# Optimization experiments

Hardware: AMD Instinct MI355X
Metric: run time of the kernel (lower is better)

The kernel has to match this reference:

```python
import jax, jax.numpy as jnp
import numpy as np

B, S, D, H = 2, 4096, 512, 8
HD = D // H  # head_dim = 64


def setup_inputs() -> dict:
    key = jax.random.key(0)
    ks = jax.random.split(key, 7)
    scale = 1.0 / np.sqrt(D)
    return {
        "x": jax.random.normal(ks[0], (B, S, D), dtype=jnp.float32),
        "Wq": jax.random.uniform(ks[1], (D, D), jnp.float32, -scale, scale),
        "bq": jax.random.uniform(ks[2], (D,), jnp.float32, -scale, scale),
        "Wk": jax.random.uniform(ks[3], (D, D), jnp.float32, -scale, scale),
        "bk": jax.random.uniform(ks[4], (D,), jnp.float32, -scale, scale),
        "Wv": jax.random.uniform(ks[5], (D, D), jnp.float32, -scale, scale),
        "bv": jax.random.uniform(ks[6], (D,), jnp.float32, -scale, scale),
    }


def reference(x, Wq, bq, Wk, bk, Wv, bv):
    # torch Linear: y = x @ W.T + b
    q = x @ Wq.T + bq  # [B,S,D]
    k = x @ Wk.T + bk
    v = x @ Wv.T + bv
    # split heads -> [B,H,S,HD]
    q = q.reshape(B, S, H, HD).transpose(0, 2, 1, 3)
    k = k.reshape(B, S, H, HD).transpose(0, 2, 1, 3)
    v = v.reshape(B, S, H, HD).transpose(0, 2, 1, 3)
    # NOTE: module scales by sqrt(pitch_dim), NOT sqrt(head_dim) -- keep faithful.
    scores = jnp.einsum("bhqd,bhkd->bhqk", q, k) / jnp.sqrt(jnp.float32(D))
    causal = jnp.tril(jnp.ones((S, S), dtype=bool))  # lower-tri incl. diag allowed
    scores = jnp.where(causal, scores, -jnp.inf)
    attn = jax.nn.softmax(scores, axis=-1)
    out = jnp.einsum("bhqk,bhkd->bhqd", attn, v)  # [B,H,S,HD]
    return out.transpose(0, 2, 1, 3).reshape(B, S, D)
```

## Files before the change

kernel.cpp:

```cpp
#include <hip/hip_runtime.h>
#include <hip/hip_bf16.h>
#include <math.h>

#define BB 2
#define SS 4096
#define DD 512
#define HH 8
#define HD 64
#define MSD (BB*SS*DD)
#define WSZ (DD*DD)

#define XOFF (4*(size_t)MSD)
#define WOFF (5*(size_t)MSD)
#define POFF (3*(size_t)MSD)

typedef __attribute__((ext_vector_type(8))) short bf16x8;
typedef __attribute__((ext_vector_type(4))) float f32x4;

__device__ __forceinline__ unsigned short f2bf(float f) {
    unsigned int u = __float_as_uint(f);
    u += 0x7fff + ((u >> 16) & 1);
    return (unsigned short)(u >> 16);
}
__device__ __forceinline__ unsigned int pk2bf(float a, float b) {
    __hip_bfloat162 h = __float22bfloat162_rn(make_float2(a, b));
    union { __hip_bfloat162 h2; unsigned int u; } cv; cv.h2 = h;
    return cv.u;
}

#define GLD16(gsrc, ldst) \
    __builtin_amdgcn_global_load_lds((const __attribute__((address_space(1))) unsigned int*)(gsrc), \
                                     (__attribute__((address_space(3))) unsigned int*)(ldst), 16, 0, 0)

#define CH(qb,t0,t1) ((unsigned)(qb) | ((unsigned)(t0)<<8) | ((unsigned)(t1)<<16))
__device__ __constant__ unsigned int SCHED[48] = {
  CH(31,0,32),  CH(31,32,64), CH(0,0,2),
  CH(15,0,32),  CH(29,0,30),  CH(1,0,4),
  CH(29,30,60), CH(14,0,30),  CH(2,0,6),
  CH(28,0,29),  CH(28,29,58), CH(3,0,8),
  CH(27,0,28),  CH(13,0,28),  CH(4,0,10),
  CH(26,0,27),  CH(26,27,54), CH(5,0,12),
  CH(25,0,26),  CH(12,0,26),  CH(6,0,14),
  CH(24,0,25),  CH(24,25,50), CH(7,0,16),
  CH(30,0,31),  CH(17,0,18),  CH(16,0,17),
  CH(30,31,62), CH(17,18,36), CH(16,17,34),
  CH(27,28,56), CH(19,0,20),  CH(8,0,18),
  CH(25,26,52), CH(20,0,21),  CH(18,0,19),
  CH(23,0,24),  CH(22,0,23),  CH(18,19,38),
  CH(23,24,48), CH(21,0,22),  CH(19,20,40),
  CH(11,0,24),  CH(21,22,44), CH(9,0,20),
  CH(22,23,46), CH(10,0,22),  CH(20,21,42),
};

__global__ __launch_bounds__(256)
void convert_bf16(const float* __restrict__ x,
                  const float* __restrict__ Wq, const float* __restrict__ Wk,
                  const float* __restrict__ Wv, unsigned short* __restrict__ ws) {
    const int i8 = blockIdx.x*256 + threadIdx.x;
    const float* src; unsigned short* dst; size_t off;
    if (i8 < MSD/8) {
        src = x; dst = ws + XOFF; off = (size_t)i8 * 8;
    } else {
        size_t o = ((size_t)i8 - MSD/8) * 8;
        int wsel = (int)(o / WSZ);
        src = (wsel == 0) ? Wq : (wsel == 1) ? Wk : Wv;
        dst = ws + WOFF + (size_t)wsel*WSZ;
        off = o % WSZ;
    }
    float4 a = *(const float4*)&src[off];
    float4 b = *(const float4*)&src[off+4];
    unsigned short r[8] = { f2bf(a.x), f2bf(a.y), f2bf(a.z), f2bf(a.w),
                            f2bf(b.x), f2bf(b.y), f2bf(b.z), f2bf(b.w) };
    *(bf16x8*)&dst[off] = *(const bf16x8*)r;
}

__global__ __launch_bounds__(512, 2)
void qkv_fused(const float* __restrict__ bq, const float* __restrict__ bk,
               const float* __restrict__ bv, unsigned short* __restrict__ ws) {
    const unsigned short* Xb = ws + XOFF;
    const unsigned short* Wz0 = ws + WOFF;
    const unsigned short* Wz1 = ws + WOFF + WSZ;
    const unsigned short* Wz2 = ws + WOFF + 2*(size_t)WSZ;

    __shared__ __align__(16) unsigned short As[2][128*64];
    __shared__ __align__(16) unsigned short Bs[3][2][128*64];

    const int tid  = threadIdx.x;
    const int w    = tid >> 6, l = tid & 63;
    const int quad = l >> 4,  r16 = l & 15;
    const int wm   = w >> 2,  wn  = w & 3;
    const int n0   = blockIdx.x * 128;
    const int m0   = blockIdx.y * 128;

    const int sr8 = l >> 3, sc = l & 7;

    f32x4 acc[3][4][2];
    #pragma unroll
    for (int z = 0; z < 3; ++z)
        #pragma unroll
        for (int i = 0; i < 4; ++i)
            #pragma unroll
            for (int j = 0; j < 2; ++j) acc[z][i][j] = (f32x4){0.f,0.f,0.f,0.f};

    auto STAGE = [&](int k0, int b) {
        #pragma unroll
        for (int u = 0; u < 2; ++u) {
            const int r0  = w*16 + u*8;
            const int row = r0 + sr8;
            const int c   = sc ^ (row & 7);
            GLD16(&Xb [(size_t)(m0 + row)*DD + k0 + c*8], &As[b][r0*64]);
            GLD16(&Wz0[(size_t)(n0 + row)*DD + k0 + c*8], &Bs[0][b][r0*64]);
            GLD16(&Wz1[(size_t)(n0 + row)*DD + k0 + c*8], &Bs[1][b][r0*64]);
            GLD16(&Wz2[(size_t)(n0 + row)*DD + k0 + c*8], &Bs[2][b][r0*64]);
        }
    };

    STAGE(0, 0);

    #pragma unroll
    for (int kt = 0; kt < 8; ++kt) {
        __syncthreads();
        if (kt + 1 < 8) STAGE((kt + 1)*64, (kt + 1) & 1);

        const int bb = kt & 1;
        #pragma unroll
        for (int kc = 0; kc < 2; ++kc) {
            bf16x8 a[4];
            #pragma unroll
            for (int i = 0; i < 4; ++i) {
                const int mr = wm*64 + i*16 + r16;
                a[i] = *(const bf16x8*)&As[bb][mr*64 + (((kc*4+quad) ^ (mr&7))*8)];
            }
            bf16x8 b0[2], b1[2], b2[2];
            #pragma unroll
            for (int j = 0; j < 2; ++j) {
                const int nr = wn*32 + j*16 + r16;
                const int sw = ((kc*4+quad) ^ (nr&7))*8;
                b0[j] = *(const bf16x8*)&Bs[0][bb][nr*64 + sw];
                b1[j] = *(const bf16x8*)&Bs[1][bb][nr*64 + sw];
                b2[j] = *(const bf16x8*)&Bs[2][bb][nr*64 + sw];
            }
            __builtin_amdgcn_s_setprio(1);
            #pragma unroll
            for (int i = 0; i < 4; ++i)
                #pragma unroll
                for (int j = 0; j < 2; ++j) {
                    acc[0][i][j] = __builtin_amdgcn_mfma_f32_16x16x32_bf16(b0[j], a[i], acc[0][i][j], 0, 0, 0);
                    acc[1][i][j] = __builtin_amdgcn_mfma_f32_16x16x32_bf16(b1[j], a[i], acc[1][i][j], 0, 0, 0);
                    acc[2][i][j] = __builtin_amdgcn_mfma_f32_16x16x32_bf16(a[i], b2[j], acc[2][i][j], 0, 0, 0);
                }
            __builtin_amdgcn_s_setprio(0);
        }
    }

    __syncthreads();
    unsigned short* Ct = &As[0][0];
    const float qscale = 0.04419417382415922f * 1.4426950408889634f;
    const float* biases[3] = { bq, bk, bv };

    #pragma unroll
    for (int z = 0; z < 3; ++z) {
        unsigned short* dst = ws + (size_t)z*MSD;
        const float* bias = biases[z];

        if (z == 2) {
            #pragma unroll
            for (int j = 0; j < 2; ++j) {
                const int nloc = wn*32 + j*16 + r16;
                const float bz = bias[n0 + nloc];
                #pragma unroll
                for (int i = 0; i < 4; ++i) {
                    const int chunk = wm*8 + i*2 + (quad>>1);
                    const int off   = (quad & 1) * 4;
                    unsigned short r4[4];
                    #pragma unroll
                    for (int reg = 0; reg < 4; ++reg)
                        r4[reg] = f2bf(acc[2][i][j][reg] + bz);
                    *(uint2*)&Ct[nloc*128 + ((chunk ^ (nloc & 7))*8) + off] = *(const uint2*)r4;
                }
            }
        } else {
            #pragma unroll
            for (int j = 0; j < 2; ++j) {
                const int nbase = wn*32 + j*16 + quad*4;
                const float4 bz4 = *(const float4*)&bias[n0 + nbase];
                const int chunk = wn*4 + j*2 + (quad>>1);
                const int off   = (quad & 1) * 4;
                #pragma unroll
                for (int i = 0; i < 4; ++i) {
                    const int mloc = wm*64 + i*16 + r16;
                    float v0 = acc[z][i][j][0] + bz4.x;
                    float v1 = acc[z][i][j][1] + bz4.y;
                    float v2 = acc[z][i][j][2] + bz4.z;
                    float v3 = acc[z][i][j][3] + bz4.w;
                    if (z == 0) { v0 *= qscale; v1 *= qscale; v2 *= qscale; v3 *= qscale; }
                    unsigned short r4[4] = { f2bf(v0), f2bf(v1), f2bf(v2), f2bf(v3) };
                    *(uint2*)&Ct[mloc*128 + ((chunk ^ (mloc & 7))*8) + off] = *(const uint2*)r4;
                }
            }
        }
        __syncthreads();

        if (z == 2) {
            const int b_ = m0 >> 12, s0_ = m0 & (SS-1);
            #pragma unroll
            for (int p = 0; p < 4; ++p) {
                const int f = p*512 + tid;
                const int nrow = f >> 4;
                const int mch  = f & 15;
                bf16x8 v = *(const bf16x8*)&Ct[nrow*128 + ((mch ^ (nrow & 7))*8)];
                const int ng = n0 + nrow;
                const int h = ng >> 6, hd = ng & 63;
                *(bf16x8*)&dst[((size_t)(b_*HH + h)*HD + hd)*SS + s0_ + mch*8] = v;
            }
        } else {
            #pragma unroll
            for (int p = 0; p < 4; ++p) {
                const int f = p*512 + tid;
                const int hh  = f >> 10;
                const int rem = f & 1023;
                const int sr  = rem >> 3;
                const int ch  = rem & 7;
                bf16x8 v = *(const bf16x8*)&Ct[sr*128 + (((hh*8 + ch) ^ (sr & 7))*8)];
                const int mg = m0 + sr;
                const int b_ = mg >> 12, s_ = mg & (SS-1);
                const int hg = (n0 >> 6) + hh;
                *(bf16x8*)&dst[((size_t)(b_*HH + hg)*SS + s_)*HD + ch*8] = v;
            }
        }
        if (z < 2) __syncthreads();
    }
}

__global__ __launch_bounds__(512, 6)
void attn_mfma(unsigned short* __restrict__ ws, float* __restrict__ out) {
    const int bx = blockIdx.x;
    const int k_ = bx >> 8;
    const int j_ = bx & 255;
    const int bh = j_ & 15;
    const int ti = j_ >> 4;
    const unsigned int e = SCHED[ti*3 + k_];
    const int qb = e & 255;
    const int t0 = (e >> 8) & 255;
    const int t1 = (e >> 16) & 255;
    const int split = !(t0 == 0 && t1 == 2*qb + 2);
    const int half  = (t0 != 0);

    const int tid  = threadIdx.x;
    const int w    = tid >> 6, l = tid & 63;
    const int quad = l >> 4,  r16 = l & 15;
    const int qlo  = qb*128 + w*16;
    const int tdiag = 2*qb + (w >> 2);
    const int qoff  = (w & 3)*16;

    const unsigned short* Qg  = ws;
    const unsigned short* Kg  = ws + (size_t)MSD;
    const unsigned short* Vtg = ws + 2*(size_t)MSD;

    __shared__ __align__(16) unsigned short Ks[2][64*64];
    __shared__ __align__(16) unsigned short Vs[2][64*64];

    const size_t kbase = (size_t)bh*SS*HD;
    const size_t vbase = (size_t)bh*HD*SS;

    bf16x8 bqf[2];
    #pragma unroll
    for (int kc = 0; kc < 2; ++kc)
        bqf[kc] = *(const bf16x8*)&Qg[kbase + (size_t)(qlo + r16)*HD + kc*32 + quad*8];

    const f32x4 ZZ = (f32x4){0.f,0.f,0.f,0.f};
    const unsigned short onep[8] = {0x3F80,0x3F80,0x3F80,0x3F80,0x3F80,0x3F80,0x3F80,0x3F80};
    const bf16x8 ones8 = *(const bf16x8*)onep;

    f32x4 od[4];
    #pragma unroll
    for (int mt = 0; mt < 4; ++mt) od[mt] = ZZ;
    f32x4 lacc = ZZ;

    const int sr8 = l >> 3, sc = l & 7;
    const int srow = w*8 + sr8;
    const int scol = sc ^ (srow & 7);

    {
        const int jb0 = t0*64;
        GLD16(&Kg [kbase + (size_t)(jb0 + srow)*HD + scol*8], &Ks[0][(w*8)*64]);
        GLD16(&Vtg[vbase + (size_t)srow*SS + jb0 + scol*8],   &Vs[0][(w*8)*64]);
    }

    for (int t = t0; t < t1; ++t) {
        __syncthreads();

        if (t + 1 < t1) {
            const int jb1 = (t + 1)*64;
            const int b1  = (t + 1 - t0) & 1;
            GLD16(&Kg [kbase + (size_t)(jb1 + srow)*HD + scol*8], &Ks[b1][(w*8)*64]);
            GLD16(&Vtg[vbase + (size_t)srow*SS + jb1 + scol*8],   &Vs[b1][(w*8)*64]);
        }

        if (t <= tdiag) {
            const int bc = (t - t0) & 1;
            const unsigned short* Kb = Ks[bc];
            const unsigned short* Vb = Vs[bc];

            f32x4 z[4];
            __builtin_amdgcn_s_setprio(1);
            #pragma unroll
            for (int mt = 0; mt < 4; ++mt) {
                const int row = mt*16 + r16;
                bf16x8 ak0 = *(const bf16x8*)&Kb[row*64 + ((quad     ^ (row&7))*8)];
                bf16x8 ak1 = *(const bf16x8*)&Kb[row*64 + (((4+quad) ^ (row&7))*8)];
                z[mt] = __builtin_amdgcn_mfma_f32_16x16x32_bf16(ak0, bqf[0], ZZ, 0, 0, 0);
                z[mt] = __builtin_amdgcn_mfma_f32_16x16x32_bf16(ak1, bqf[1], z[mt], 0, 0, 0);
            }
            __builtin_amdgcn_s_setprio(0);

            if (t == tdiag) {
                #pragma unroll
                for (int mt = 0; mt < 4; ++mt)
                    #pragma unroll
                    for (int reg = 0; reg < 4; ++reg)
                        if (mt*16 + quad*4 + reg > qoff + r16)
                            z[mt][reg] = -1e30f;
            }

            unsigned int X0[4], X1[4];
            #pragma unroll
            for (int mt = 0; mt < 4; ++mt) {
                X0[mt] = pk2bf(__builtin_amdgcn_exp2f(z[mt][0]),
                               __builtin_amdgcn_exp2f(z[mt][1]));
                X1[mt] = pk2bf(__builtin_amdgcn_exp2f(z[mt][2]),
                               __builtin_amdgcn_exp2f(z[mt][3]));
            }

            bf16x8 pf[2];
            #pragma unroll
            for (int kc = 0; kc < 2; ++kc) {
                unsigned int a0 = X0[2*kc], b0 = X0[2*kc+1];
                unsigned int a1 = X1[2*kc], b1 = X1[2*kc+1];
                asm("v_permlane32_swap_b32 %0, %1" : "+v"(a0), "+v"(b0));
                asm("v_permlane16_swap_b32 %0, %1" : "+v"(a0), "+v"(b0));
                asm("v_permlane32_swap_b32 %0, %1" : "+v"(a1), "+v"(b1));
                asm("v_permlane16_swap_b32 %0, %1" : "+v"(a1), "+v"(b1));
                unsigned int wv[4] = { a0, a1, b0, b1 };
                pf[kc] = *(const bf16x8*)wv;
            }

            __builtin_amdgcn_s_setprio(1);
            lacc = __builtin_amdgcn_mfma_f32_16x16x32_bf16(ones8, pf[0], lacc, 0, 0, 0);
            lacc = __builtin_amdgcn_mfma_f32_16x16x32_bf16(ones8, pf[1], lacc, 0, 0, 0);
            #pragma unroll
            for (int mt = 0; mt < 4; ++mt) {
                const int row = mt*16 + r16;
                bf16x8 av0 = *(const bf16x8*)&Vb[row*64 + ((quad     ^ (row&7))*8)];
                bf16x8 av1 = *(const bf16x8*)&Vb[row*64 + (((4+quad) ^ (row&7))*8)];
                od[mt] = __builtin_amdgcn_mfma_f32_16x16x32_bf16(av0, pf[0], od[mt], 0, 0, 0);
                od[mt] = __builtin_amdgcn_mfma_f32_16x16x32_bf16(av1, pf[1], od[mt], 0, 0, 0);
            }
            __builtin_amdgcn_s_setprio(0);
        }
    }

    if (split) {
        const int p = 2*(bh*16 + (qb - 16)) + half;
        float* Op = (float*)(ws + POFF) + (size_t)p*(128*64);
        float* Lp = (float*)(ws + WOFF) + p*128;
        const int qloc = w*16 + r16;
        if (quad == 0) Lp[qloc] = lacc[0];
        #pragma unroll
        for (int mt = 0; mt < 4; ++mt)
            *(f32x4*)&Op[(size_t)qloc*64 + mt*16 + quad*4] = od[mt];
    } else {
        const int b_ = bh >> 3, h = bh & 7;
        const float inv = 1.0f / lacc[0];
        const int q = qlo + r16;
        float* op = out + ((size_t)(b_*SS + q))*DD + h*HD;
        #pragma unroll
        for (int mt = 0; mt < 4; ++mt) {
            float4 tt;
            tt.x = od[mt][0]*inv; tt.y = od[mt][1]*inv;
            tt.z = od[mt][2]*inv; tt.w = od[mt][3]*inv;
            *(float4*)&op[mt*16 + quad*4] = tt;
        }
    }
}

__global__ __launch_bounds__(256)
void attn_combine(const unsigned short* __restrict__ ws, float* __restrict__ out) {
    const int i  = blockIdx.x*256 + threadIdx.x;
    const int d4 = i & 15;
    const int q  = (i >> 4) & 127;
    const int r  = i >> 11;
    const int bh = r >> 4, qb = 16 + (r & 15);

    const float* Opart = (const float*)(ws + POFF);
    const float* Lpart = (const float*)(ws + WOFF);

    const float4 a = *(const float4*)&Opart[((size_t)(2*r)*128 + q)*64 + d4*4];
    const float4 b = *(const float4*)&Opart[((size_t)(2*r + 1)*128 + q)*64 + d4*4];
    const float lt = Lpart[(2*r)*128 + q] + Lpart[(2*r + 1)*128 + q];
    const float inv = 1.0f / lt;

    const int qg = qb*128 + q;
    const int b_ = bh >> 3, h = bh & 7;
    float4 o;
    o.x = (a.x + b.x)*inv; o.y = (a.y + b.y)*inv;
    o.z = (a.z + b.z)*inv; o.w = (a.w + b.w)*inv;
    *(float4*)&out[((size_t)(b_*SS + qg))*DD + h*HD + d4*4] = o;
}

extern "C" void kernel_launch(void* const* d_in, const int* in_sizes, int n_in,
                              void* d_out, int out_size, void* d_ws, size_t ws_size,
                              hipStream_t stream) {
    const float* x  = (const float*)d_in[0];
    const float* Wq = (const float*)d_in[1];
    const float* bq = (const float*)d_in[2];
    const float* Wk = (const float*)d_in[3];
    const float* bk = (const float*)d_in[4];
    const float* Wv = (const float*)d_in[5];
    const float* bv = (const float*)d_in[6];
    float* out = (float*)d_out;
    unsigned short* ws = (unsigned short*)d_ws;

    const int nconv = (MSD/8 + 3*WSZ/8 + 255) / 256;
    convert_bf16<<<nconv, 256, 0, stream>>>(x, Wq, Wk, Wv, ws);

    dim3 ggrid(DD/128, (BB*SS)/128);
    qkv_fused<<<ggrid, 512, 0, stream>>>(bq, bk, bv, ws);

    attn_mfma<<<768, 512, 0, stream>>>(ws, out);
    attn_combine<<<2048, 256, 0, stream>>>(ws, out);
}
```

Baseline: 152.2 us.

## Give each attention wave two query tiles and halve block size to 256

The attention kernel now uses 4 waves per block instead of 8, and each wave handles 32 query rows as two 16-row tiles instead of one. Each K and V fragment read from LDS is reused for two MFMA tiles, which halves LDS reads per FLOP, and each thread issues two global-to-LDS loads per tile. The cost is more accumulator and P registers per wave and fewer waves to hide latency. The launch bounds change to 256 threads with a minimum of 4 blocks per CU.

```diff
diff --git a/kernel.cpp b/kernel.cpp
--- a/kernel.cpp
+++ b/kernel.cpp
@@ -232,7 +232,7 @@
     }
 }
 
-__global__ __launch_bounds__(512, 6)
+__global__ __launch_bounds__(256, 4)
 void attn_mfma(unsigned short* __restrict__ ws, float* __restrict__ out) {
     const int bx = blockIdx.x;
     const int k_ = bx >> 8;
@@ -249,9 +249,9 @@
     const int tid  = threadIdx.x;
     const int w    = tid >> 6, l = tid & 63;
     const int quad = l >> 4,  r16 = l & 15;
-    const int qlo  = qb*128 + w*16;
-    const int tdiag = 2*qb + (w >> 2);
-    const int qoff  = (w & 3)*16;
+    const int qlo  = qb*128 + w*32;
+    const int tdiag = 2*qb + (w >> 1);
+    const int qoff  = 32*(w & 1);
 
     const unsigned short* Qg  = ws;
     const unsigned short* Kg  = ws + (size_t)MSD;
@@ -263,28 +263,35 @@
     const size_t kbase = (size_t)bh*SS*HD;
     const size_t vbase = (size_t)bh*HD*SS;
 
-    bf16x8 bqf[2];
+    bf16x8 bqf[2][2];
     #pragma unroll
-    for (int kc = 0; kc < 2; ++kc)
-        bqf[kc] = *(const bf16x8*)&Qg[kbase + (size_t)(qlo + r16)*HD + kc*32 + quad*8];
+    for (int nt = 0; nt < 2; ++nt)
+        #pragma unroll
+        for (int kc = 0; kc < 2; ++kc)
+            bqf[nt][kc] = *(const bf16x8*)&Qg[kbase + (size_t)(qlo + nt*16 + r16)*HD + kc*32 + quad*8];
 
     const f32x4 ZZ = (f32x4){0.f,0.f,0.f,0.f};
     const unsigned short onep[8] = {0x3F80,0x3F80,0x3F80,0x3F80,0x3F80,0x3F80,0x3F80,0x3F80};
     const bf16x8 ones8 = *(const bf16x8*)onep;
 
-    f32x4 od[4];
+    f32x4 od[4][2];
     #pragma unroll
-    for (int mt = 0; mt < 4; ++mt) od[mt] = ZZ;
-    f32x4 lacc = ZZ;
+    for (int mt = 0; mt < 4; ++mt)
+        #pragma unroll
+        for (int nt = 0; nt < 2; ++nt) od[mt][nt] = ZZ;
+    f32x4 lacc[2] = {ZZ, ZZ};
 
     const int sr8 = l >> 3, sc = l & 7;
-    const int srow = w*8 + sr8;
-    const int scol = sc ^ (srow & 7);
 
     {
         const int jb0 = t0*64;
-        GLD16(&Kg [kbase + (size_t)(jb0 + srow)*HD + scol*8], &Ks[0][(w*8)*64]);
-        GLD16(&Vtg[vbase + (size_t)srow*SS + jb0 + scol*8],   &Vs[0][(w*8)*64]);
+        #pragma unroll
+        for (int u = 0; u < 2; ++u) {
+            const int row = w*16 + u*8 + sr8;
+            const int c   = sc ^ (row & 7);
+            GLD16(&Kg [kbase + (size_t)(jb0 + row)*HD + c*8], &Ks[0][(w*16 + u*8)*64]);
+            GLD16(&Vtg[vbase + (size_t)row*SS + jb0 + c*8],   &Vs[0][(w*16 + u*8)*64]);
+        }
     }
 
     for (int t = t0; t < t1; ++t) {
@@ -293,8 +300,13 @@
         if (t + 1 < t1) {
             const int jb1 = (t + 1)*64;
             const int b1  = (t + 1 - t0) & 1;
-            GLD16(&Kg [kbase + (size_t)(jb1 + srow)*HD + scol*8], &Ks[b1][(w*8)*64]);
-            GLD16(&Vtg[vbase + (size_t)srow*SS + jb1 + scol*8],   &Vs[b1][(w*8)*64]);
+            #pragma unroll
+            for (int u = 0; u < 2; ++u) {
+                const int row = w*16 + u*8 + sr8;
+                const int c   = sc ^ (row & 7);
+                GLD16(&Kg [kbase + (size_t)(jb1 + row)*HD + c*8], &Ks[b1][(w*16 + u*8)*64]);
+                GLD16(&Vtg[vbase + (size_t)row*SS + jb1 + c*8],   &Vs[b1][(w*16 + u*8)*64]);
+            }
         }
 
         if (t <= tdiag) {
@@ -302,15 +314,18 @@
             const unsigned short* Kb = Ks[bc];
             const unsigned short* Vb = Vs[bc];
 
-            f32x4 z[4];
+            f32x4 z[4][2];
             __builtin_amdgcn_s_setprio(1);
             #pragma unroll
             for (int mt = 0; mt < 4; ++mt) {
                 const int row = mt*16 + r16;
                 bf16x8 ak0 = *(const bf16x8*)&Kb[row*64 + ((quad     ^ (row&7))*8)];
                 bf16x8 ak1 = *(const bf16x8*)&Kb[row*64 + (((4+quad) ^ (row&7))*8)];
-                z[mt] = __builtin_amdgcn_mfma_f32_16x16x32_bf16(ak0, bqf[0], ZZ, 0, 0, 0);
-                z[mt] = __builtin_amdgcn_mfma_f32_16x16x32_bf16(ak1, bqf[1], z[mt], 0, 0, 0);
+                #pragma unroll
+                for (int nt = 0; nt < 2; ++nt) {
+                    z[mt][nt] = __builtin_amdgcn_mfma_f32_16x16x32_bf16(ak0, bqf[nt][0], ZZ, 0, 0, 0);
+                    z[mt][nt] = __builtin_amdgcn_mfma_f32_16x16x32_bf16(ak1, bqf[nt][1], z[mt][nt], 0, 0, 0);
+                }
             }
             __builtin_amdgcn_s_setprio(0);
 
@@ -318,43 +333,55 @@
                 #pragma unroll
                 for (int mt = 0; mt < 4; ++mt)
                     #pragma unroll
-                    for (int reg = 0; reg < 4; ++reg)
-                        if (mt*16 + quad*4 + reg > qoff + r16)
-                            z[mt][reg] = -1e30f;
-            }
-
-            unsigned int X0[4], X1[4];
-            #pragma unroll
-            for (int mt = 0; mt < 4; ++mt) {
-                X0[mt] = pk2bf(__builtin_amdgcn_exp2f(z[mt][0]),
-                               __builtin_amdgcn_exp2f(z[mt][1]));
-                X1[mt] = pk2bf(__builtin_amdgcn_exp2f(z[mt][2]),
-                               __builtin_amdgcn_exp2f(z[mt][3]));
-            }
-
-            bf16x8 pf[2];
-            #pragma unroll
-            for (int kc = 0; kc < 2; ++kc) {
-                unsigned int a0 = X0[2*kc], b0 = X0[2*kc+1];
-                unsigned int a1 = X1[2*kc], b1 = X1[2*kc+1];
-                asm("v_permlane32_swap_b32 %0, %1" : "+v"(a0), "+v"(b0));
-                asm("v_permlane16_swap_b32 %0, %1" : "+v"(a0), "+v"(b0));
-                asm("v_permlane32_swap_b32 %0, %1" : "+v"(a1), "+v"(b1));
-                asm("v_permlane16_swap_b32 %0, %1" : "+v"(a1), "+v"(b1));
-                unsigned int wv[4] = { a0, a1, b0, b1 };
-                pf[kc] = *(const bf16x8*)wv;
-            }
+                    for (int nt = 0; nt < 2; ++nt)
+                        #pragma unroll
+                        for (int reg = 0; reg < 4; ++reg)
+                            if (mt*16 + quad*4 + reg > qoff + nt*16 + r16)
+                                z[mt][nt][reg] = -1e30f;
+            }
+
+            unsigned int X0[4][2], X1[4][2];
+            #pragma unroll
+            for (int mt = 0; mt < 4; ++mt)
+                #pragma unroll
+                for (int nt = 0; nt < 2; ++nt) {
+                    X0[mt][nt] = pk2bf(__builtin_amdgcn_exp2f(z[mt][nt][0]),
+                                       __builtin_amdgcn_exp2f(z[mt][nt][1]));
+                    X1[mt][nt] = pk2bf(__builtin_amdgcn_exp2f(z[mt][nt][2]),
+                                       __builtin_amdgcn_exp2f(z[mt][nt][3]));
+                }
+
+            bf16x8 pf[2][2];
+            #pragma unroll
+            for (int nt = 0; nt < 2; ++nt)
+                #pragma unroll
+                for (int kc = 0; kc < 2; ++kc) {
+                    unsigned int a0 = X0[2*kc][nt], b0 = X0[2*kc+1][nt];
+                    unsigned int a1 = X1[2*kc][nt], b1 = X1[2*kc+1][nt];
+                    asm("v_permlane32_swap_b32 %0, %1" : "+v"(a0), "+v"(b0));
+                    asm("v_permlane16_swap_b32 %0, %1" : "+v"(a0), "+v"(b0));
+                    asm("v_permlane32_swap_b32 %0, %1" : "+v"(a1), "+v"(b1));
+                    asm("v_permlane16_swap_b32 %0, %1" : "+v"(a1), "+v"(b1));
+                    unsigned int wv[4] = { a0, a1, b0, b1 };
+                    pf[nt][kc] = *(const bf16x8*)wv;
+                }
 
             __builtin_amdgcn_s_setprio(1);
-            lacc = __builtin_amdgcn_mfma_f32_16x16x32_bf16(ones8, pf[0], lacc, 0, 0, 0);
-            lacc = __builtin_amdgcn_mfma_f32_16x16x32_bf16(ones8, pf[1], lacc, 0, 0, 0);
+            #pragma unroll
+            for (int nt = 0; nt < 2; ++nt) {
+                lacc[nt] = __builtin_amdgcn_mfma_f32_16x16x32_bf16(ones8, pf[nt][0], lacc[nt], 0, 0, 0);
+                lacc[nt] = __builtin_amdgcn_mfma_f32_16x16x32_bf16(ones8, pf[nt][1], lacc[nt], 0, 0, 0);
+            }
             #pragma unroll
             for (int mt = 0; mt < 4; ++mt) {
                 const int row = mt*16 + r16;
                 bf16x8 av0 = *(const bf16x8*)&Vb[row*64 + ((quad     ^ (row&7))*8)];
                 bf16x8 av1 = *(const bf16x8*)&Vb[row*64 + (((4+quad) ^ (row&7))*8)];
-                od[mt] = __builtin_amdgcn_mfma_f32_16x16x32_bf16(av0, pf[0], od[mt], 0, 0, 0);
-                od[mt] = __builtin_amdgcn_mfma_f32_16x16x32_bf16(av1, pf[1], od[mt], 0, 0, 0);
+                #pragma unroll
+                for (int nt = 0; nt < 2; ++nt) {
+                    od[mt][nt] = __builtin_amdgcn_mfma_f32_16x16x32_bf16(av0, pf[nt][0], od[mt][nt], 0, 0, 0);
+                    od[mt][nt] = __builtin_amdgcn_mfma_f32_16x16x32_bf16(av1, pf[nt][1], od[mt][nt], 0, 0, 0);
+                }
             }
             __builtin_amdgcn_s_setprio(0);
         }
@@ -364,22 +391,28 @@
         const int p = 2*(bh*16 + (qb - 16)) + half;
         float* Op = (float*)(ws + POFF) + (size_t)p*(128*64);
         float* Lp = (float*)(ws + WOFF) + p*128;
-        const int qloc = w*16 + r16;
-        if (quad == 0) Lp[qloc] = lacc[0];
-        #pragma unroll
-        for (int mt = 0; mt < 4; ++mt)
-            *(f32x4*)&Op[(size_t)qloc*64 + mt*16 + quad*4] = od[mt];
+        #pragma unroll
+        for (int nt = 0; nt < 2; ++nt) {
+            const int qloc = w*32 + nt*16 + r16;
+            if (quad == 0) Lp[qloc] = lacc[nt][0];
+            #pragma unroll
+            for (int mt = 0; mt < 4; ++mt)
+                *(f32x4*)&Op[(size_t)qloc*64 + mt*16 + quad*4] = od[mt][nt];
+        }
     } else {
         const int b_ = bh >> 3, h = bh & 7;
-        const float inv = 1.0f / lacc[0];
-        const int q = qlo + r16;
-        float* op = out + ((size_t)(b_*SS + q))*DD + h*HD;
-        #pragma unroll
-        for (int mt = 0; mt < 4; ++mt) {
-            float4 tt;
-            tt.x = od[mt][0]*inv; tt.y = od[mt][1]*inv;
-            tt.z = od[mt][2]*inv; tt.w = od[mt][3]*inv;
-            *(float4*)&op[mt*16 + quad*4] = tt;
+        #pragma unroll
+        for (int nt = 0; nt < 2; ++nt) {
+            const float inv = 1.0f / lacc[nt][0];
+            const int q = qlo + nt*16 + r16;
+            float* op = out + ((size_t)(b_*SS + q))*DD + h*HD;
+            #pragma unroll
+            for (int mt = 0; mt < 4; ++mt) {
+                float4 tt;
+                tt.x = od[mt][nt][0]*inv; tt.y = od[mt][nt][1]*inv;
+                tt.z = od[mt][nt][2]*inv; tt.w = od[mt][nt][3]*inv;
+                *(float4*)&op[mt*16 + quad*4] = tt;
+            }
         }
     }
 }
@@ -427,6 +460,6 @@
     dim3 ggrid(DD/128, (BB*SS)/128);
     qkv_fused<<<ggrid, 512, 0, stream>>>(bq, bk, bv, ws);
 
-    attn_mfma<<<768, 512, 0, stream>>>(ws, out);
+    attn_mfma<<<768, 256, 0, stream>>>(ws, out);
     attn_combine<<<2048, 256, 0, stream>>>(ws, out);
 }
```

Measured after the change: 151.1 us. No clear change (-0.7%).
